# Performance work log

Hardware: AMD Instinct MI355X
Metric: run time of the kernel (lower is better)

Reference implementation:

```python
import jax, jax.numpy as jnp
import numpy as np
from math import sqrt

NUM_HEADS = 8
HIDDEN = 768
ATTN_DIM = HIDDEN // NUM_HEADS  # 96
NEG = -1e10


def setup_inputs() -> dict:
    key = jax.random.key(0)
    ks = jax.random.split(key, 6)
    b, s, dim = 8, 1024, 768
    scale = 1.0 / sqrt(dim)
    return {
        "span_embeddings": jax.random.normal(ks[0], (b, s, dim), dtype=jnp.float32),
        "span_tags": jax.random.randint(ks[1], (b, s), 0, 5),
        "w_weight": jax.random.normal(ks[2], (1, dim), dtype=jnp.float32) * scale,
        "w_q": jax.random.normal(ks[3], (HIDDEN, dim), dtype=jnp.float32) * scale,
        "w_k": jax.random.normal(ks[4], (HIDDEN, dim), dtype=jnp.float32) * scale,
        "w_v": jax.random.normal(ks[5], (HIDDEN, dim), dtype=jnp.float32) * scale,
    }


def reference(span_embeddings, span_tags, w_weight, w_q, w_k, w_v):
    b, s, _ = span_embeddings.shape
    pad = span_tags == 0  # [b, s]

    # additive span attention weights: Linear(dim -> 1), mask padded, softmax over seq
    attn_weights = span_embeddings @ w_weight.T  # [b, s, 1]
    attn_weights = jnp.where(pad[:, :, None], NEG, attn_weights)
    attn_weights = jax.nn.softmax(attn_weights, axis=1)

    # NOTE: original views hidden as (attn_dim, num_heads) in that order
    qs = (span_embeddings @ w_q.T).reshape(b, s, ATTN_DIM, NUM_HEADS)
    ks = (span_embeddings @ w_k.T).reshape(b, s, ATTN_DIM, NUM_HEADS)
    vs = (span_embeddings @ w_v.T).reshape(b, s, ATTN_DIM, NUM_HEADS)

    rel = jnp.einsum('bqdh,bkdh->bqkh', qs, ks) / sqrt(ATTN_DIM)  # [b,q,k,h]
    # original masks along query axis (relevance_weights[span_tags.eq(0)] = NEG)
    rel = jnp.where(pad[:, :, None, None], NEG, rel)
    # original softmax(dim=-1) -> over the HEADS axis (faithful quirk)
    rel = jax.nn.softmax(rel, axis=-1)

    span_value = jnp.einsum('bqkh,bkdh->bqdh', rel, vs).reshape(b, s, HIDDEN)
    weighted_value = jnp.sum(attn_weights * span_value, axis=1)  # [b, hidden]
    return weighted_value
```

## Files before the change

kernel.cpp:

```cpp
#include <hip/hip_runtime.h>
#include <hip/hip_bf16.h>
#include <math.h>

#define NEGV (-1e10f)

typedef __attribute__((ext_vector_type(8))) short bf16x8;
typedef __attribute__((ext_vector_type(4))) float f32x4;
typedef __attribute__((ext_vector_type(16))) float f32x16;

static __device__ __forceinline__ unsigned short f2bf(float f) {
  unsigned int u = __builtin_bit_cast(unsigned int, f);
  unsigned int r = (u + 0x7fffu + ((u >> 16) & 1u)) >> 16;
  return (unsigned short)r;
}
static __device__ __forceinline__ float bf2f(unsigned short v) {
  return __builtin_bit_cast(float, (unsigned int)v << 16);
}
static __device__ __forceinline__ unsigned int pkbf(float lo, float hi) {
  unsigned int r;
  asm("v_cvt_pk_bf16_f32 %0, %1, %2" : "=v"(r) : "v"(lo), "v"(hi));
  return r;
}

#define GLD16(g, l)                                                   \
  __builtin_amdgcn_global_load_lds(                                   \
      (const __attribute__((address_space(1))) void*)(g),             \
      (__attribute__((address_space(3))) void*)(l), 16, 0, 0)

__global__ __launch_bounds__(256) void cast_inputs(
    const float* __restrict__ emb, const int* __restrict__ tags,
    const float* __restrict__ ww, const float* __restrict__ wq,
    const float* __restrict__ wk, const float* __restrict__ wv,
    unsigned short* __restrict__ embbf, float* __restrict__ logits,
    unsigned short* __restrict__ wbf, float* __restrict__ out) {
  int bx = blockIdx.x;
  if (bx < 2048) {
    int w = threadIdx.x >> 6, lane = threadIdx.x & 63;
    int row = bx * 4 + w;
    const float4* src = (const float4*)(emb + (size_t)row * 768);
    const float4* wsrc = (const float4*)ww;
    uint2* dst = (uint2*)(embbf + (size_t)row * 768);
    float d = 0.f;
#pragma unroll
    for (int j = 0; j < 3; j++) {
      int idx = lane + 64 * j;
      float4 v = src[idx];
      float4 wv = wsrc[idx];
      d += v.x * wv.x + v.y * wv.y + v.z * wv.z + v.w * wv.w;
      uint2 o;
      o.x = pkbf(v.x, v.y);
      o.y = pkbf(v.z, v.w);
      dst[idx] = o;
    }
#pragma unroll
    for (int off = 32; off; off >>= 1) d += __shfl_xor(d, off);
    if (lane == 0) logits[row] = (tags[row] == 0) ? NEGV : d;
  } else {
    int g = bx - 2048;
    int z = g / 576;
    int idx = (g - z * 576) * 256 + threadIdx.x;
    const float* src = (z == 0) ? wq : (z == 1) ? wk : wv;
    float4 v = ((const float4*)src)[idx];
    if (z == 0) {
      const float C2 = 0.10206207261596577f * 1.4426950408889634f;
      v.x *= C2; v.y *= C2; v.z *= C2; v.w *= C2;
    }
    uint2 o;
    o.x = pkbf(v.x, v.y);
    o.y = pkbf(v.z, v.w);
    uint2* W2 = (uint2*)(wbf + (size_t)z * 589824);
    if (z == 2) {
      W2[idx] = o;
    } else {
      int f = idx / 192;
      int col4 = idx - f * 192;
      int h = f & 7, dg = f >> 3;
      int tt = dg >> 4, ddl = dg & 15;
      int wn = ddl >> 3, cb = (ddl >> 2) & 1, j = ddl & 3;
      int orow = tt * 128 + wn * 64 + j * 16 + cb * 8 + h;
      W2[orow * 192 + col4] = o;
    }
    if (bx == 3775) {
      float4 z4 = {0.f, 0.f, 0.f, 0.f};
#pragma unroll
      for (int q = 0; q < 6; q++) ((float4*)out)[q * 256 + threadIdx.x] = z4;
    }
  }
}

__global__ __launch_bounds__(256, 3) void qkv_gemm(
    const unsigned short* __restrict__ A, const unsigned short* __restrict__ Wbf,
    unsigned short* __restrict__ Qf, unsigned short* __restrict__ Kf,
    unsigned short* __restrict__ Vbf) {
  __shared__ __align__(16) unsigned short sm[24576];
  int g = blockIdx.x;
  int xcd = g & 7, local = g >> 3;
  int mbi = xcd * 8 + (local & 7);
  int nbz = local >> 3;
  int z = nbz / 6;
  int nbi = nbz - z * 6;
  const unsigned short* B = Wbf + (size_t)z * 589824;
  int mb = mbi * 128, nb = nbi * 128;
  int tid = threadIdx.x;
  int w = tid >> 6, lane = tid & 63;
  int wm = w >> 1, wn = w & 1;
  int c = lane & 15, quad = lane >> 4;
  int lrow = lane >> 2;
  int lcol = ((lane & 3) ^ ((lrow >> 1) & 3)) * 8;
  const unsigned short* Ag = A + (size_t)(mb + w * 32 + lrow) * 768 + lcol;
  const unsigned short* Bg = B + (size_t)(nb + w * 32 + lrow) * 768 + lcol;
  int woff = w * 1024;

#define PREFETCH(buf, kb)                                                   \
  do {                                                                      \
    GLD16(Ag + (kb), sm + (buf) * 8192 + woff);                             \
    GLD16(Ag + (kb) + 16 * 768, sm + (buf) * 8192 + woff + 512);            \
    GLD16(Bg + (kb), sm + (buf) * 8192 + 4096 + woff);                      \
    GLD16(Bg + (kb) + 16 * 768, sm + (buf) * 8192 + 4096 + woff + 512);     \
  } while (0)

  f32x4 acc[4][4];
#pragma unroll
  for (int i = 0; i < 4; i++)
#pragma unroll
    for (int j = 0; j < 4; j++) acc[i][j] = 0;

  PREFETCH(0, 0);
  PREFETCH(1, 32);

  int rd = 0;
  int sw = (quad ^ ((c >> 1) & 3)) * 8;
  for (int it = 0; it < 24; it++) {
    if (it < 23) {
      asm volatile("s_waitcnt vmcnt(4) lgkmcnt(0)" ::: "memory");
    } else {
      asm volatile("s_waitcnt vmcnt(0) lgkmcnt(0)" ::: "memory");
    }
    __builtin_amdgcn_s_barrier();
    if (it + 2 < 24) {
      int wr = rd + 2;
      if (wr >= 3) wr -= 3;
      PREFETCH(wr, (it + 2) * 32);
    }
    const unsigned short* Ab = sm + rd * 8192;
    const unsigned short* Bb = Ab + 4096;
    bf16x8 af[4], bfr[4];
#pragma unroll
    for (int i = 0; i < 4; i++)
      af[i] = *(const bf16x8*)&Ab[(wm * 64 + i * 16 + c) * 32 + sw];
#pragma unroll
    for (int j = 0; j < 4; j++)
      bfr[j] = *(const bf16x8*)&Bb[(wn * 64 + j * 16 + c) * 32 + sw];
#pragma unroll
    for (int i = 0; i < 4; i++)
#pragma unroll
      for (int j = 0; j < 4; j++)
        acc[i][j] = __builtin_amdgcn_mfma_f32_16x16x32_bf16(af[i], bfr[j],
                                                            acc[i][j], 0, 0, 0);
    rd = (rd == 2) ? 0 : rd + 1;
  }
  __syncthreads();

  if (z == 2) {
#pragma unroll
    for (int i = 0; i < 4; i++)
#pragma unroll
      for (int j = 0; j < 4; j++)
#pragma unroll
        for (int r = 0; r < 4; r++) {
          int rl = wm * 64 + i * 16 + quad * 4 + r;
          int cl = wn * 64 + j * 16 + c;
          sm[rl * 136 + cl] = f2bf(acc[i][j][r]);
        }
    __syncthreads();
#pragma unroll
    for (int it2 = 0; it2 < 8; it2++) {
      int g2 = it2 * 256 + tid;
      int rl = g2 >> 4;
      int cu = (g2 & 15) * 8;
      bf16x8 vdat = *(const bf16x8*)&sm[rl * 136 + cu];
      *(bf16x8*)&Vbf[(size_t)(mb + rl) * 768 + nb + cu] = vdat;
    }
  } else {
    unsigned short* O = (z == 0) ? Qf : Kf;
#pragma unroll
    for (int i = 0; i < 4; i++) {
#pragma unroll
      for (int r = 0; r < 4; r++) {
        int qlr = wm * 64 + i * 16 + quad * 4 + r;
        int chunkL = (qlr >> 5) * 8 + (c & 7);
        int lane32 = (qlr & 31) + wn * 32;
        uint2 o;
        o.x = pkbf(acc[i][0][r], acc[i][1][r]);
        o.y = pkbf(acc[i][2][r], acc[i][3][r]);
        *(uint2*)&sm[chunkL * 520 + lane32 * 8 + 4 * (c >> 3)] = o;
      }
    }
    __syncthreads();
    int bq = mb >> 10;
    int qt32g0 = (mb & 1023) >> 5;
    int tt = nbi;
#pragma unroll
    for (int it2 = 0; it2 < 8; it2++) {
      int gg = it2 * 256 + tid;
      int chunkL = gg >> 6;
      int off = (gg & 63) * 8;
      bf16x8 vdat = *(const bf16x8*)&sm[chunkL * 520 + off];
      int qt32 = qt32g0 + (chunkL >> 3), h = chunkL & 7;
      size_t dst = ((((size_t)(bq * 32 + qt32) * 8 + h) * 6 + tt) << 9) + off;
      *(bf16x8*)&O[dst] = vdat;
    }
  }
#undef PREFETCH
}

__global__ __launch_bounds__(256) void attn(
    const unsigned short* __restrict__ Qf, const unsigned short* __restrict__ Kf,
    const float* __restrict__ logits, float* __restrict__ Ptp) {
  __shared__ float pbuf[1024];
  __shared__ float red[4];
  int id = blockIdx.x;
  int b = id & 7, qb = (id >> 3) & 15, kb = id >> 7;
  int tid = threadIdx.x, w = tid >> 6, lane = tid & 63;
  int wq = w >> 1, wk = w & 1;
  const unsigned short* Qb =
      Qf + ((size_t)(b * 32 + qb * 2 + wq) * 48) * 512 + (size_t)lane * 8;
  const unsigned short* Kb =
      Kf + ((size_t)(b * 32 + kb * 2 + wk) * 48) * 512 + (size_t)lane * 8;

  bf16x8 qa[6], ka[6];
#pragma unroll
  for (int t = 0; t < 6; t++) {
    qa[t] = *(const bf16x8*)(Qb + (size_t)t * 512);
    ka[t] = *(const bf16x8*)(Kb + (size_t)t * 512);
  }

  {
    const float* L = logits + b * 1024;
    float x0 = L[tid], x1 = L[tid + 256], x2 = L[tid + 512], x3 = L[tid + 768];
    float m = fmaxf(fmaxf(x0, x1), fmaxf(x2, x3));
#pragma unroll
    for (int off = 32; off; off >>= 1) m = fmaxf(m, __shfl_xor(m, off));
    if ((tid & 63) == 0) red[tid >> 6] = m;
    __syncthreads();
    m = fmaxf(fmaxf(red[0], red[1]), fmaxf(red[2], red[3]));
    float e0 = __expf(x0 - m), e1 = __expf(x1 - m), e2 = __expf(x2 - m),
          e3 = __expf(x3 - m);
    float s = e0 + e1 + e2 + e3;
#pragma unroll
    for (int off = 32; off; off >>= 1) s += __shfl_xor(s, off);
    __syncthreads();
    if ((tid & 63) == 0) red[tid >> 6] = s;
    __syncthreads();
    float inv = 1.0f / (red[0] + red[1] + red[2] + red[3]);
    pbuf[tid] = e0 * inv;
    pbuf[tid + 256] = e1 * inv;
    pbuf[tid + 512] = e2 * inv;
    pbuf[tid + 768] = e3 * inv;
    __syncthreads();
  }

  f32x16 acc[8];
#pragma unroll
  for (int h = 0; h < 8; h++) acc[h] = 0;
#pragma unroll
  for (int h = 0; h < 8; h++) {
#pragma unroll
    for (int t = 0; t < 6; t++) {
      bf16x8 a = (h == 0) ? qa[t] : *(const bf16x8*)(Qb + (size_t)(h * 6 + t) * 512);
      bf16x8 bb = (h == 0) ? ka[t] : *(const bf16x8*)(Kb + (size_t)(h * 6 + t) * 512);
      acc[h] = __builtin_amdgcn_mfma_f32_32x32x16_bf16(a, bb, acc[h], 0, 0, 0);
    }
  }

  float awv[16];
#pragma unroll
  for (int reg = 0; reg < 16; reg++) {
    int row = (reg & 3) + 8 * (reg >> 2) + 4 * (lane >> 5);
    awv[reg] = pbuf[qb * 64 + wq * 32 + row];
  }
  __syncthreads();
  float partial[8];
#pragma unroll
  for (int h = 0; h < 8; h++) partial[h] = 0.f;
#pragma unroll
  for (int reg = 0; reg < 16; reg++) {
    float v[8];
    float ssum = 0.f;
#pragma unroll
    for (int h = 0; h < 8; h++) {
      float e = exp2f(acc[h][reg]);
      v[h] = e;
      ssum += e;
    }
    float g = awv[reg] * __builtin_amdgcn_rcpf(ssum);
#pragma unroll
    for (int h = 0; h < 8; h++) partial[h] += v[h] * g;
  }
#pragma unroll
  for (int h = 0; h < 8; h++) {
    float v = partial[h];
    v += __shfl_xor(v, 32);
    partial[h] = v;
  }
  if (lane < 32) {
#pragma unroll
    for (int h = 0; h < 8; h++) pbuf[w * 256 + lane * 8 + h] = partial[h];
  }
  __syncthreads();
#pragma unroll
  for (int wk2 = 0; wk2 < 2; wk2++) {
    float s = pbuf[wk2 * 256 + tid] + pbuf[(2 + wk2) * 256 + tid];
    int kcol = tid >> 3, h = tid & 7;
    Ptp[(((size_t)qb * 8 + b) * 1024 + kb * 64 + wk2 * 32 + kcol) * 8 + h] = s;
  }
}

__global__ __launch_bounds__(256) void finalize(
    const float* __restrict__ Ptp, const unsigned short* __restrict__ Vbf,
    float* __restrict__ out) {
  __shared__ float ps[256];
  int kc = blockIdx.x, b = blockIdx.y;
  int t = threadIdx.x;
  {
    int k = kc * 32 + (t >> 3), h = t & 7;
    float s = 0.f;
#pragma unroll
    for (int qc = 0; qc < 16; qc++)
      s += Ptp[(((size_t)qc * 8 + b) * 1024 + k) * 8 + h];
    ps[t] = s;
  }
  __syncthreads();
  if (t < 192) {
    int o0 = t * 4;
    int hb = o0 & 7;
    float a0 = 0, a1 = 0, a2 = 0, a3 = 0;
    const unsigned short* Vb = Vbf + ((size_t)b * 1024 + kc * 32) * 768 + o0;
#pragma unroll 4
    for (int kk = 0; kk < 32; kk++) {
      ushort4 vv = *(const ushort4*)(Vb + (size_t)kk * 768);
      const float* p = &ps[kk * 8 + hb];
      a0 += p[0] * bf2f(vv.x);
      a1 += p[1] * bf2f(vv.y);
      a2 += p[2] * bf2f(vv.z);
      a3 += p[3] * bf2f(vv.w);
    }
    atomicAdd(&out[b * 768 + o0], a0);
    atomicAdd(&out[b * 768 + o0 + 1], a1);
    atomicAdd(&out[b * 768 + o0 + 2], a2);
    atomicAdd(&out[b * 768 + o0 + 3], a3);
  }
}

extern "C" void kernel_launch(void* const* d_in, const int* in_sizes, int n_in,
                              void* d_out, int out_size, void* d_ws,
                              size_t ws_size, hipStream_t stream) {
  const float* emb = (const float*)d_in[0];
  const int* tags = (const int*)d_in[1];
  const float* ww = (const float*)d_in[2];
  const float* wq = (const float*)d_in[3];
  const float* wk = (const float*)d_in[4];
  const float* wv = (const float*)d_in[5];
  float* out = (float*)d_out;
  char* ws = (char*)d_ws;
  unsigned short* embbf = (unsigned short*)(ws + 0);
  unsigned short* wbf   = (unsigned short*)(ws + 12582912);
  unsigned short* Qf    = (unsigned short*)(ws + 16121856);
  unsigned short* Kf    = (unsigned short*)(ws + 28704768);
  unsigned short* Vbf   = (unsigned short*)(ws + 41287680);
  float* logits         = (float*)(ws + 53870592);
  float* Ptp            = (float*)(ws + 53936128);

  cast_inputs<<<3776, 256, 0, stream>>>(emb, tags, ww, wq, wk, wv, embbf,
                                        logits, wbf, out);
  qkv_gemm<<<1152, 256, 0, stream>>>(embbf, wbf, Qf, Kf, Vbf);
  attn<<<2048, 256, 0, stream>>>(Qf, Kf, logits, Ptp);
  finalize<<<dim3(32, 8), 256, 0, stream>>>(Ptp, Vbf, out);
}
```

Before: 159.7 us.

## Stage Q/K tiles through LDS with triple-buffered async global-to-LDS loads

The attn kernel used to load Q and K fragments for each head straight from global memory into registers. It now streams them per head into a three-slot LDS ring using global_load_lds, keeping two heads in flight ahead of the MFMA loop and coordinating with vmcnt waits and barriers. The logits softmax preamble overlaps with the first two prefetches, and its __syncthreads are replaced by lighter lgkmcnt barriers. This adds about 72KB of LDS per block, which can reduce occupancy, plus extra barriers on every head iteration.

```diff
diff --git a/kernel.cpp b/kernel.cpp
--- a/kernel.cpp
+++ b/kernel.cpp
@@ -26,6 +26,12 @@
   __builtin_amdgcn_global_load_lds(                                   \
       (const __attribute__((address_space(1))) void*)(g),             \
       (__attribute__((address_space(3))) void*)(l), 16, 0, 0)
+
+#define LBAR()                                                  \
+  do {                                                          \
+    asm volatile("s_waitcnt lgkmcnt(0)" ::: "memory");          \
+    __builtin_amdgcn_s_barrier();                               \
+  } while (0)
 
 __global__ __launch_bounds__(256) void cast_inputs(
     const float* __restrict__ emb, const int* __restrict__ tags,
@@ -217,61 +223,96 @@
 __global__ __launch_bounds__(256) void attn(
     const unsigned short* __restrict__ Qf, const unsigned short* __restrict__ Kf,
     const float* __restrict__ logits, float* __restrict__ Ptp) {
+  __shared__ __align__(16) unsigned short kv[36864];
   __shared__ float pbuf[1024];
   __shared__ float red[4];
   int id = blockIdx.x;
   int b = id & 7, qb = (id >> 3) & 15, kb = id >> 7;
   int tid = threadIdx.x, w = tid >> 6, lane = tid & 63;
   int wq = w >> 1, wk = w & 1;
-  const unsigned short* Qb =
-      Qf + ((size_t)(b * 32 + qb * 2 + wq) * 48) * 512 + (size_t)lane * 8;
-  const unsigned short* Kb =
-      Kf + ((size_t)(b * 32 + kb * 2 + wk) * 48) * 512 + (size_t)lane * 8;
-
-  bf16x8 qa[6], ka[6];
-#pragma unroll
-  for (int t = 0; t < 6; t++) {
-    qa[t] = *(const bf16x8*)(Qb + (size_t)t * 512);
-    ka[t] = *(const bf16x8*)(Kb + (size_t)t * 512);
-  }
+
+  const float* L = logits + b * 1024;
+  float x0 = L[tid], x1 = L[tid + 256], x2 = L[tid + 512], x3 = L[tid + 768];
+
+  const unsigned short* srcp[6];
+  int dsto[6];
+#pragma unroll
+  for (int l6 = 0; l6 < 6; l6++) {
+    int cch = l6 * 4 + w;
+    int part = (cch >= 12) ? 1 : 0;
+    int r = cch - part * 12;
+    int qt = r / 6, t = r - qt * 6;
+    const unsigned short* base = part ? Kf : Qf;
+    int tb = part ? kb : qb;
+    srcp[l6] = base + ((size_t)((b * 32 + tb * 2 + qt) * 8) * 6 + t) * 512 +
+               lane * 8;
+    dsto[l6] = cch * 512 + lane * 8;
+  }
+
+#define STAGE(slot, hh)                                          \
+  do {                                                           \
+    GLD16(srcp[0] + (hh) * 3072, kv + (slot) * 12288 + dsto[0]); \
+    GLD16(srcp[1] + (hh) * 3072, kv + (slot) * 12288 + dsto[1]); \
+    GLD16(srcp[2] + (hh) * 3072, kv + (slot) * 12288 + dsto[2]); \
+    GLD16(srcp[3] + (hh) * 3072, kv + (slot) * 12288 + dsto[3]); \
+    GLD16(srcp[4] + (hh) * 3072, kv + (slot) * 12288 + dsto[4]); \
+    GLD16(srcp[5] + (hh) * 3072, kv + (slot) * 12288 + dsto[5]); \
+  } while (0)
+
+  STAGE(0, 0);
+  STAGE(1, 1);
 
   {
-    const float* L = logits + b * 1024;
-    float x0 = L[tid], x1 = L[tid + 256], x2 = L[tid + 512], x3 = L[tid + 768];
     float m = fmaxf(fmaxf(x0, x1), fmaxf(x2, x3));
 #pragma unroll
     for (int off = 32; off; off >>= 1) m = fmaxf(m, __shfl_xor(m, off));
     if ((tid & 63) == 0) red[tid >> 6] = m;
-    __syncthreads();
+    LBAR();
     m = fmaxf(fmaxf(red[0], red[1]), fmaxf(red[2], red[3]));
     float e0 = __expf(x0 - m), e1 = __expf(x1 - m), e2 = __expf(x2 - m),
           e3 = __expf(x3 - m);
     float s = e0 + e1 + e2 + e3;
 #pragma unroll
     for (int off = 32; off; off >>= 1) s += __shfl_xor(s, off);
-    __syncthreads();
+    LBAR();
     if ((tid & 63) == 0) red[tid >> 6] = s;
-    __syncthreads();
+    LBAR();
     float inv = 1.0f / (red[0] + red[1] + red[2] + red[3]);
     pbuf[tid] = e0 * inv;
     pbuf[tid + 256] = e1 * inv;
     pbuf[tid + 512] = e2 * inv;
     pbuf[tid + 768] = e3 * inv;
-    __syncthreads();
   }
 
   f32x16 acc[8];
 #pragma unroll
   for (int h = 0; h < 8; h++) acc[h] = 0;
+
+  int rd = 0;
 #pragma unroll
   for (int h = 0; h < 8; h++) {
+    if (h < 7) {
+      asm volatile("s_waitcnt vmcnt(6) lgkmcnt(0)" ::: "memory");
+    } else {
+      asm volatile("s_waitcnt vmcnt(0) lgkmcnt(0)" ::: "memory");
+    }
+    __builtin_amdgcn_s_barrier();
+    if (h + 2 < 8) {
+      int wr = rd + 2;
+      if (wr >= 3) wr -= 3;
+      STAGE(wr, h + 2);
+    }
+    const unsigned short* Qs = kv + rd * 12288 + wq * 3072 + lane * 8;
+    const unsigned short* Ks = kv + rd * 12288 + 6144 + wk * 3072 + lane * 8;
 #pragma unroll
     for (int t = 0; t < 6; t++) {
-      bf16x8 a = (h == 0) ? qa[t] : *(const bf16x8*)(Qb + (size_t)(h * 6 + t) * 512);
-      bf16x8 bb = (h == 0) ? ka[t] : *(const bf16x8*)(Kb + (size_t)(h * 6 + t) * 512);
+      bf16x8 a = *(const bf16x8*)(Qs + t * 512);
+      bf16x8 bb = *(const bf16x8*)(Ks + t * 512);
       acc[h] = __builtin_amdgcn_mfma_f32_32x32x16_bf16(a, bb, acc[h], 0, 0, 0);
     }
-  }
+    rd = (rd == 2) ? 0 : rd + 1;
+  }
+#undef STAGE
 
   float awv[16];
 #pragma unroll
```

Result: slower. 164.7 us (+3.1%).
